# Kernel optimization log

Hardware: AMD Instinct MI355X
Metric: run time of the kernel (lower is better)

## Reference

```python
import jax, jax.numpy as jnp
import numpy as np


def conv2d(x, w, b):
    pad = (w.shape[-1] - 1) // 2
    y = jax.lax.conv_general_dilated(x, w, (1, 1), [(pad, pad), (pad, pad)],
                                     dimension_numbers=('NCHW', 'OIHW', 'NCHW'))
    return y + b[None, :, None, None]


def mish(x):
    return x * jnp.tanh(jax.nn.softplus(x))


def setup_inputs() -> dict:
    key = jax.random.key(0)
    ks = jax.random.split(key, 8)
    B, C, H, W = 8, 16, 256, 256
    s = 0.1
    return dict(
        x=jax.random.normal(ks[0], (B, C, H, W), jnp.float32),
        W1=jax.random.normal(ks[1], (4, 1, 3, 3), jnp.float32) * s,      # conv1: 1->4, k=3
        b1=jnp.zeros((4,), jnp.float32),
        Wred=jax.random.normal(ks[2], (1, 4, 1, 1), jnp.float32) * s,    # involution reduce 4->1
        bred=jnp.zeros((1,), jnp.float32),
        Wspan=jax.random.normal(ks[3], (9, 1, 1, 1), jnp.float32) * s,   # involution span 1->k^2
        bspan=jnp.zeros((9,), jnp.float32),
        W2=jax.random.normal(ks[4], (C, 4 * C, 3, 3), jnp.float32) * s,  # conv2: 4C->C, k=3
        b2=jnp.zeros((C,), jnp.float32),
        Weca=jax.random.normal(ks[5], (3,), jnp.float32) * s,            # ECA 1D conv kernel
    )


def reference(x, W1, b1, Wred, bred, Wspan, bspan, W2, b2, Weca):
    B, C, H, W = x.shape
    H2 = H // 2
    K2 = 9  # 3x3 involution kernel
    # per-channel 1->4 conv + Mish: vectorize the Python channel loop by folding C into batch
    xs = x.reshape(B * C, 1, H, W)
    f = mish(conv2d(xs, W1, b1))                      # (B*C, 4, H, W)
    top, bot = f[:, :, :H2], f[:, :, H2:]             # each (B*C, 4, H2, W)
    # involution2(y1, y2): dynamic per-pixel 3x3 kernel from bottom half, applied to top half
    ker = conv2d(jax.nn.relu(conv2d(bot, Wred, bred)), Wspan, bspan)   # (B*C, 9, H2, W)
    patches = jax.lax.conv_general_dilated_patches(
        top, (3, 3), (1, 1), [(1, 1), (1, 1)],
        dimension_numbers=('NCHW', 'OIHW', 'NCHW'))                    # (B*C, 4*9, H2, W), channel-major
    patches = patches.reshape(B * C, 4, K2, H2, W)
    top_inv = (patches * ker[:, None]).sum(axis=2)                     # (B*C, 4, H2, W)
    # shuffle/concat: out channel-block i = [inv_top_i ; bottom_{(i+1) % C}] along height
    ti = top_inv.reshape(B, C, 4, H2, W)
    bo = bot.reshape(B, C, 4, H2, W)
    shuffled = jnp.concatenate([ti, jnp.roll(bo, -1, axis=1)], axis=3)  # (B, C, 4, H, W)
    shuffled = shuffled.reshape(B, 4 * C, H, W)
    out = mish(conv2d(shuffled, W2, b2))               # (B, C, H, W)
    # ECA: gate from global-avg-pooled `out`, 1D cross-correlation (k=3, pad=1) over channels
    pooled = out.mean(axis=(2, 3))                     # (B, C)
    yp = jnp.pad(pooled, ((0, 0), (1, 1)))
    gate = jax.nn.sigmoid(Weca[0] * yp[:, :-2] + Weca[1] * yp[:, 1:-1] + Weca[2] * yp[:, 2:])
    return x * gate[:, :, None, None]
```

## Files before the change

### kernel.cpp

```cpp
#include <hip/hip_runtime.h>
#include <hip/hip_bf16.h>

#define H 256
#define Wd 256
#define H2 128

typedef unsigned short ushort_t;
typedef __attribute__((ext_vector_type(8))) short short8;
typedef __attribute__((ext_vector_type(4))) float f32x4;
typedef __attribute__((ext_vector_type(2))) float f32x2;

__device__ __forceinline__ float mishf(float v){
  if (v > 15.f) return v;
  float e = __expf(v);
  float w = e*(e+2.f);
  return v * w * __builtin_amdgcn_rcpf(w + 2.f);
}

__device__ __forceinline__ ushort_t f2bf(float f){
  unsigned int u = __float_as_uint(f);
  u += 0x7fffu + ((u >> 16) & 1u);
  return (ushort_t)(u >> 16);
}
__device__ __forceinline__ float bf2f(ushort_t h){
  return __uint_as_float(((unsigned int)h) << 16);
}


__global__ void k0_pack(const float* __restrict__ W2, ushort_t* __restrict__ wpack)
{
  int idx = blockIdx.x*128 + threadIdx.x;
  if (idx >= 1152) return;
  int lane  = idx & 63;
  int s     = (idx >> 6) % 9;
  int khalf = idx / 576;
  int n = lane & 15, g = lane >> 4;
  unsigned int w[4];
#pragma unroll
  for (int h = 0; h < 4; ++h){
    int ch0 = khalf*32 + g*8 + 2*h;
    unsigned lo = f2bf(W2[(n*64 + ch0  )*9 + s]);
    unsigned hi = f2bf(W2[(n*64 + ch0+1)*9 + s]);
    w[h] = lo | (hi << 16);
  }
  *(uint4*)(wpack + (size_t)idx*8) = make_uint4(w[0], w[1], w[2], w[3]);
}

__global__ __launch_bounds__(256) void k12(
    const float* __restrict__ x, const float* __restrict__ W1,
    const float* __restrict__ b1, const float* __restrict__ Wred,
    const float* __restrict__ bred, const float* __restrict__ Wspan,
    const float* __restrict__ bspan, ushort_t* __restrict__ shuf)
{
  __shared__ float xt[20][69];
  __shared__ float xb[18][69];
  __shared__ float ft[4][18][69];

  int bid = blockIdx.x;
  int n   = bid >> 5;
  int t   = bid & 31;
  int itop0 = (t >> 2) * 16;
  int j0    = (t & 3) * 64;
  int tid = threadIdx.x;
  const float* xp = x + (size_t)n * (H*Wd);

  f32x2 w01[9], w23[9], b01, b23, wspb[9];
  float wredr[4];
  float bredr = bred[0];
#pragma unroll
  for (int k=0;k<9;k++){
    w01[k] = f32x2{W1[k], W1[9+k]};
    w23[k] = f32x2{W1[18+k], W1[27+k]};
    wspb[k] = f32x2{Wspan[k], bspan[k]};
  }
  b01 = f32x2{b1[0], b1[1]};
  b23 = f32x2{b1[2], b1[3]};
#pragma unroll
  for (int m=0;m<4;m++) wredr[m] = Wred[m];

  for (int idx=tid; idx<20*68; idx+=256){
    int r = idx/68, c = idx - r*68;
    int row = itop0-2+r, col = j0-2+c;
    xt[r][c] = (row>=0 && col>=0 && col<Wd) ? xp[row*Wd+col] : 0.f;
  }
  for (int idx=tid; idx<18*68; idx+=256){
    int r = idx/68, c = idx - r*68;
    int row = 127+itop0+r, col = j0-2+c;
    xb[r][c] = (row<H && col>=0 && col<Wd) ? xp[row*Wd+col] : 0.f;
  }
  __syncthreads();

  for (int idx=tid; idx<18*66; idx+=256){
    int r = idx/66, c = idx - r*66;
    int frow = itop0-1+r, fcol = j0-1+c;
    bool ok = (frow>=0 && frow<H2 && fcol>=0 && fcol<Wd);
    f32x2 s01 = b01, s23 = b23;
#pragma unroll
    for (int ky=0;ky<3;ky++)
#pragma unroll
      for (int kx=0;kx<3;kx++){
        float xv = xt[r+ky][c+kx];
        f32x2 xv2 = f32x2{xv, xv};
        s01 = xv2*w01[ky*3+kx] + s01;
        s23 = xv2*w23[ky*3+kx] + s23;
      }
    ft[0][r][c] = ok ? mishf(s01.x) : 0.f;
    ft[1][r][c] = ok ? mishf(s01.y) : 0.f;
    ft[2][r][c] = ok ? mishf(s23.x) : 0.f;
    ft[3][r][c] = ok ? mishf(s23.y) : 0.f;
  }

  int lr  = tid >> 4;
  int lc4 = (tid & 15) * 4;
  int trow = itop0 + lr;
  int bq = n >> 4, cq = n & 15;

  float fb[4][4];
  {
    float xv[3][6];
#pragma unroll
    for (int r=0;r<3;r++)
#pragma unroll
      for (int c=0;c<6;c++)
        xv[r][c] = xb[lr+r][lc4+1+c];
#pragma unroll
    for (int p=0;p<4;p++){
      f32x2 s01 = b01, s23 = b23;
#pragma unroll
      for (int ky=0;ky<3;ky++)
#pragma unroll
        for (int kx=0;kx<3;kx++){
          float v = xv[ky][p+kx];
          f32x2 v2 = f32x2{v, v};
          s01 = v2*w01[ky*3+kx] + s01;
          s23 = v2*w23[ky*3+kx] + s23;
        }
      fb[0][p] = mishf(s01.x); fb[1][p] = mishf(s01.y);
      fb[2][p] = mishf(s23.x); fb[3][p] = mishf(s23.y);
    }
  }
  int cdst = (cq + 15) & 15;
  size_t bbase = ((size_t)(bq*16 + cdst))*65536 + (size_t)(128+trow)*256 + j0 + lc4;
#pragma unroll
  for (int p=0;p<4;p++){
    ushort4 hv;
    hv.x = f2bf(fb[0][p]); hv.y = f2bf(fb[1][p]);
    hv.z = f2bf(fb[2][p]); hv.w = f2bf(fb[3][p]);
    *(ushort4*)(shuf + (bbase + p)*4) = hv;
  }
  float gv[4];
#pragma unroll
  for (int p=0;p<4;p++){
    float s = bredr;
#pragma unroll
    for (int m=0;m<4;m++) s = fmaf(fb[m][p], wredr[m], s);
    gv[p] = fmaxf(s, 0.f);
  }

  __syncthreads();

  float o[4][4];
#pragma unroll
  for (int m=0;m<4;m++){
    float fv[3][6];
#pragma unroll
    for (int ky=0;ky<3;ky++)
#pragma unroll
      for (int c=0;c<6;c++)
        fv[ky][c] = ft[m][lr+ky][lc4+c];
#pragma unroll
    for (int p=0;p<4;p++){
      f32x2 ab = f32x2{0.f, 0.f};
#pragma unroll
      for (int ky=0;ky<3;ky++)
#pragma unroll
        for (int kx=0;kx<3;kx++){
          float fvv = fv[ky][p+kx];
          ab = f32x2{fvv, fvv}*wspb[ky*3+kx] + ab;
        }
      o[m][p] = fmaf(gv[p], ab.x, ab.y);
    }
  }
  size_t pbase = ((size_t)(bq*16 + cq))*65536 + (size_t)trow*256 + j0 + lc4;
#pragma unroll
  for (int p=0;p<4;p++){
    ushort4 hv;
    hv.x = f2bf(o[0][p]); hv.y = f2bf(o[1][p]);
    hv.z = f2bf(o[2][p]); hv.w = f2bf(o[3][p]);
    *(ushort4*)(shuf + (pbase + p)*4) = hv;
  }
}

__global__ __launch_bounds__(256) void k3_conv2(
    const ushort_t* __restrict__ shuf, const ushort_t* __restrict__ wpack,
    const float* __restrict__ b2, float* __restrict__ scratch)
{
  __shared__ f32x4 mg[2][8][64];
  __shared__ float pacc[16];

  int bid0 = blockIdx.x;
  int bid  = (bid0 & 7)*256 + (bid0 >> 3);
  int b   = bid >> 8;
  int t   = bid & 255;
  int rb  = t >> 3;
  int cb  = t & 7;
  int tid = threadIdx.x;
  int lane = tid & 63;
  int n = lane & 15;
  int g = lane >> 4;
  int wid = tid >> 6;
  int colhalf = wid & 1;
  int khalf   = wid >> 1;

  if (tid < 16) pacc[tid] = 0.f;

  const short8* wp = (const short8*)wpack + (size_t)khalf*576 + lane;
  short8 afr[9];
#pragma unroll
  for (int s = 0; s < 9; ++s) afr[s] = wp[s*64];

  f32x4 acc[8];
#pragma unroll
  for (int r = 0; r < 8; ++r) acc[r] = f32x4{0.f,0.f,0.f,0.f};

  int r0 = rb*8 - 1;
  int c  = cb*32 - 1 + colhalf*16 + n;
  int p0 = khalf*8 + g*2;
  const ushort_t* sp = shuf + ((size_t)(b*16 + p0))*262144;

#pragma unroll
  for (int hr = 0; hr < 10; ++hr){
    int grow = r0 + hr;
    bool rok = (unsigned)grow < 256u;
    uint2 va[3], vb[3];
#pragma unroll
    for (int kx = 0; kx < 3; ++kx){
      int gcol = c + kx;
      uint2 a = make_uint2(0u,0u), bv = make_uint2(0u,0u);
      if (rok && (unsigned)gcol < 256u){
        const ushort_t* pp = sp + (size_t)(grow*256 + gcol)*4;
        a  = *(const uint2*)pp;
        bv = *(const uint2*)(pp + 262144);
      }
      va[kx] = a; vb[kx] = bv;
    }
#pragma unroll
    for (int kx = 0; kx < 3; ++kx){
      union { uint4 u; short8 s; } cv;
      cv.u = make_uint4(va[kx].x, va[kx].y, vb[kx].x, vb[kx].y);
#pragma unroll
      for (int ky = 0; ky < 3; ++ky){
        int orow = hr - ky;
        if (orow >= 0 && orow < 8){
          acc[orow] = __builtin_amdgcn_mfma_f32_16x16x32_bf16(
              afr[ky*3+kx], cv.s, acc[orow], 0, 0, 0);
        }
      }
    }
  }

  if (khalf == 1){
#pragma unroll
    for (int r = 0; r < 8; ++r) mg[colhalf][r][lane] = acc[r];
  }
  __syncthreads();

  if (khalf == 0){
    float b2v[4];
#pragma unroll
    for (int q = 0; q < 4; ++q) b2v[q] = b2[g*4 + q];
    float po[4] = {0.f, 0.f, 0.f, 0.f};
#pragma unroll
    for (int r = 0; r < 8; ++r){
      f32x4 o = acc[r] + mg[colhalf][r][lane];
#pragma unroll
      for (int q = 0; q < 4; ++q) po[q] += mishf(o[q] + b2v[q]);
    }
#pragma unroll
    for (int q = 0; q < 4; ++q){
#pragma unroll
      for (int mk = 1; mk < 16; mk <<= 1) po[q] += __shfl_xor(po[q], mk);
    }
    if (n == 0){
#pragma unroll
      for (int q = 0; q < 4; ++q) atomicAdd(&pacc[g*4 + q], po[q]);
    }
  }
  __syncthreads();
  if (tid < 16) scratch[bid*16 + tid] = pacc[tid];
}

__global__ void k4_gate(const float* __restrict__ scratch,
                        const float* __restrict__ Weca,
                        float* __restrict__ gate)
{
  __shared__ float rr[16][16];
  __shared__ float pool[16];
  int b = blockIdx.x;
  int t = threadIdx.x;
  int oc = t & 15, ch = t >> 4;
  float s = 0.f;
  for (int u = 0; u < 16; ++u)
    s += scratch[(size_t)(b*256 + ch*16 + u)*16 + oc];
  rr[ch][oc] = s;
  __syncthreads();
  if (t < 16){
    float tot = 0.f;
#pragma unroll
    for (int k = 0; k < 16; ++k) tot += rr[k][t];
    pool[t] = tot * (1.0f/65536.0f);
  }
  __syncthreads();
  if (t < 16){
    float pm = (t > 0)  ? pool[t-1] : 0.f;
    float p0 = pool[t];
    float pp = (t < 15) ? pool[t+1] : 0.f;
    float z = Weca[0]*pm + Weca[1]*p0 + Weca[2]*pp;
    gate[b*16 + t] = 1.f/(1.f + __expf(-z));
  }
}

__global__ __launch_bounds__(256) void k5_scale(
    const f32x4* __restrict__ x4, const float* __restrict__ gate,
    f32x4* __restrict__ out4)
{
  int idx = blockIdx.x*256 + threadIdx.x;
  float g = gate[idx >> 14];
  f32x4 v = x4[idx] * g;
  __builtin_nontemporal_store(v, &out4[idx]);
}

extern "C" void kernel_launch(void* const* d_in, const int* in_sizes, int n_in,
                              void* d_out, int out_size, void* d_ws, size_t ws_size,
                              hipStream_t stream)
{
  const float* x     = (const float*)d_in[0];
  const float* W1    = (const float*)d_in[1];
  const float* b1    = (const float*)d_in[2];
  const float* Wred  = (const float*)d_in[3];
  const float* bred  = (const float*)d_in[4];
  const float* Wspan = (const float*)d_in[5];
  const float* bspan = (const float*)d_in[6];
  const float* W2    = (const float*)d_in[7];
  const float* b2    = (const float*)d_in[8];
  const float* Weca  = (const float*)d_in[9];

  ushort_t* shuf    = (ushort_t*)d_ws;
  float*    gate    = (float*)((char*)d_ws + 67108864);
  ushort_t* wpack   = (ushort_t*)((char*)d_ws + 67108864 + 1024);
  float*    scratch = (float*)d_out;

  k0_pack<<<9, 128, 0, stream>>>(W2, wpack);
  k12    <<<4096, 256, 0, stream>>>(x, W1, b1, Wred, bred, Wspan, bspan, shuf);
  k3_conv2<<<2048, 256, 0, stream>>>(shuf, wpack, b2, scratch);
  k4_gate<<<8, 256, 0, stream>>>(scratch, Weca, gate);
  k5_scale<<<8192, 256, 0, stream>>>((const f32x4*)x, gate, (f32x4*)d_out);
}
```

Before: 90.61 us.

## Vectorize k12 global loads/stores and store top features as packed bf16 in LDS

The input tile loads now use float4 reads with a shifted 4-aligned halo, and the shuffle-buffer writes are widened to two 16-byte stores per thread. The intermediate mish features for the top half are kept in shared memory as packed bf16 pairs, which halves LDS footprint and read traffic. The involution loop is reordered to load the packed features once and unpack them for all four channels. This adds bf16 rounding of intermediate features before the involution, a small precision change, in exchange for lower LDS pressure and fewer memory instructions.

```diff
diff --git a/kernel.cpp b/kernel.cpp
--- a/kernel.cpp
+++ b/kernel.cpp
@@ -24,6 +24,15 @@
 }
 __device__ __forceinline__ float bf2f(ushort_t h){
   return __uint_as_float(((unsigned int)h) << 16);
+}
+__device__ __forceinline__ unsigned packbf(float a, float b){
+  return (unsigned)f2bf(a) | ((unsigned)f2bf(b) << 16);
+}
+__device__ __forceinline__ float lo16(unsigned u){
+  return __uint_as_float(u << 16);
+}
+__device__ __forceinline__ float hi16(unsigned u){
+  return __uint_as_float(u & 0xffff0000u);
 }
 
 
@@ -52,9 +61,9 @@
     const float* __restrict__ bred, const float* __restrict__ Wspan,
     const float* __restrict__ bspan, ushort_t* __restrict__ shuf)
 {
-  __shared__ float xt[20][69];
-  __shared__ float xb[18][69];
-  __shared__ float ft[4][18][69];
+  __shared__ float xt[20][73];
+  __shared__ float xb[18][73];
+  __shared__ unsigned ftp[2][18][69];
 
   int bid = blockIdx.x;
   int n   = bid >> 5;
@@ -78,36 +87,46 @@
 #pragma unroll
   for (int m=0;m<4;m++) wredr[m] = Wred[m];
 
-  for (int idx=tid; idx<20*68; idx+=256){
-    int r = idx/68, c = idx - r*68;
-    int row = itop0-2+r, col = j0-2+c;
-    xt[r][c] = (row>=0 && col>=0 && col<Wd) ? xp[row*Wd+col] : 0.f;
-  }
-  for (int idx=tid; idx<18*68; idx+=256){
-    int r = idx/68, c = idx - r*68;
-    int row = 127+itop0+r, col = j0-2+c;
-    xb[r][c] = (row<H && col>=0 && col<Wd) ? xp[row*Wd+col] : 0.f;
+  for (int idx=tid; idx<360; idx+=256){
+    int r = idx/18, q = idx - r*18;
+    int grow = itop0-2+r, gcol = j0-4+q*4;
+    float4 v = make_float4(0.f,0.f,0.f,0.f);
+    if (grow>=0 && gcol>=0 && gcol<Wd)
+      v = *(const float4*)(xp + (size_t)grow*Wd + gcol);
+    int c0 = q*4;
+    xt[r][c0] = v.x; xt[r][c0+1] = v.y; xt[r][c0+2] = v.z; xt[r][c0+3] = v.w;
+  }
+  for (int idx=tid; idx<324; idx+=256){
+    int r = idx/18, q = idx - r*18;
+    int grow = 127+itop0+r, gcol = j0-4+q*4;
+    float4 v = make_float4(0.f,0.f,0.f,0.f);
+    if (grow<H && gcol>=0 && gcol<Wd)
+      v = *(const float4*)(xp + (size_t)grow*Wd + gcol);
+    int c0 = q*4;
+    xb[r][c0] = v.x; xb[r][c0+1] = v.y; xb[r][c0+2] = v.z; xb[r][c0+3] = v.w;
   }
   __syncthreads();
 
   for (int idx=tid; idx<18*66; idx+=256){
     int r = idx/66, c = idx - r*66;
     int frow = itop0-1+r, fcol = j0-1+c;
-    bool ok = (frow>=0 && frow<H2 && fcol>=0 && fcol<Wd);
-    f32x2 s01 = b01, s23 = b23;
-#pragma unroll
-    for (int ky=0;ky<3;ky++)
-#pragma unroll
-      for (int kx=0;kx<3;kx++){
-        float xv = xt[r+ky][c+kx];
-        f32x2 xv2 = f32x2{xv, xv};
-        s01 = xv2*w01[ky*3+kx] + s01;
-        s23 = xv2*w23[ky*3+kx] + s23;
-      }
-    ft[0][r][c] = ok ? mishf(s01.x) : 0.f;
-    ft[1][r][c] = ok ? mishf(s01.y) : 0.f;
-    ft[2][r][c] = ok ? mishf(s23.x) : 0.f;
-    ft[3][r][c] = ok ? mishf(s23.y) : 0.f;
+    unsigned u01 = 0u, u23 = 0u;
+    if (frow>=0 && frow<H2 && fcol>=0 && fcol<Wd){
+      f32x2 s01 = b01, s23 = b23;
+#pragma unroll
+      for (int ky=0;ky<3;ky++)
+#pragma unroll
+        for (int kx=0;kx<3;kx++){
+          float xv = xt[r+ky][c+kx+2];
+          f32x2 xv2 = f32x2{xv, xv};
+          s01 = xv2*w01[ky*3+kx] + s01;
+          s23 = xv2*w23[ky*3+kx] + s23;
+        }
+      u01 = packbf(mishf(s01.x), mishf(s01.y));
+      u23 = packbf(mishf(s23.x), mishf(s23.y));
+    }
+    ftp[0][r][c] = u01;
+    ftp[1][r][c] = u23;
   }
 
   int lr  = tid >> 4;
@@ -122,7 +141,7 @@
     for (int r=0;r<3;r++)
 #pragma unroll
       for (int c=0;c<6;c++)
-        xv[r][c] = xb[lr+r][lc4+1+c];
+        xv[r][c] = xb[lr+r][lc4+3+c];
 #pragma unroll
     for (int p=0;p<4;p++){
       f32x2 s01 = b01, s23 = b23;
@@ -141,12 +160,13 @@
   }
   int cdst = (cq + 15) & 15;
   size_t bbase = ((size_t)(bq*16 + cdst))*65536 + (size_t)(128+trow)*256 + j0 + lc4;
-#pragma unroll
-  for (int p=0;p<4;p++){
-    ushort4 hv;
-    hv.x = f2bf(fb[0][p]); hv.y = f2bf(fb[1][p]);
-    hv.z = f2bf(fb[2][p]); hv.w = f2bf(fb[3][p]);
-    *(ushort4*)(shuf + (bbase + p)*4) = hv;
+  {
+    unsigned w0 = packbf(fb[0][0], fb[1][0]), w1 = packbf(fb[2][0], fb[3][0]);
+    unsigned w2 = packbf(fb[0][1], fb[1][1]), w3 = packbf(fb[2][1], fb[3][1]);
+    *(uint4*)(shuf + bbase*4) = make_uint4(w0,w1,w2,w3);
+    unsigned w4 = packbf(fb[0][2], fb[1][2]), w5 = packbf(fb[2][2], fb[3][2]);
+    unsigned w6 = packbf(fb[0][3], fb[1][3]), w7 = packbf(fb[2][3], fb[3][3]);
+    *(uint4*)(shuf + (bbase+2)*4) = make_uint4(w4,w5,w6,w7);
   }
   float gv[4];
 #pragma unroll
@@ -159,35 +179,44 @@
 
   __syncthreads();
 
+  unsigned fv0[3][6], fv1[3][6];
+#pragma unroll
+  for (int ky=0;ky<3;ky++)
+#pragma unroll
+    for (int c=0;c<6;c++){
+      fv0[ky][c] = ftp[0][lr+ky][lc4+c];
+      fv1[ky][c] = ftp[1][lr+ky][lc4+c];
+    }
+
   float o[4][4];
 #pragma unroll
-  for (int m=0;m<4;m++){
-    float fv[3][6];
+  for (int p=0;p<4;p++){
+    f32x2 ab0 = f32x2{0.f,0.f}, ab1 = ab0, ab2 = ab0, ab3 = ab0;
 #pragma unroll
     for (int ky=0;ky<3;ky++)
 #pragma unroll
-      for (int c=0;c<6;c++)
-        fv[ky][c] = ft[m][lr+ky][lc4+c];
-#pragma unroll
-    for (int p=0;p<4;p++){
-      f32x2 ab = f32x2{0.f, 0.f};
-#pragma unroll
-      for (int ky=0;ky<3;ky++)
-#pragma unroll
-        for (int kx=0;kx<3;kx++){
-          float fvv = fv[ky][p+kx];
-          ab = f32x2{fvv, fvv}*wspb[ky*3+kx] + ab;
-        }
-      o[m][p] = fmaf(gv[p], ab.x, ab.y);
-    }
+      for (int kx=0;kx<3;kx++){
+        f32x2 w = wspb[ky*3+kx];
+        unsigned u0 = fv0[ky][p+kx], u1 = fv1[ky][p+kx];
+        float a = lo16(u0), b = hi16(u0), c2 = lo16(u1), d = hi16(u1);
+        ab0 = f32x2{a,a}*w + ab0;
+        ab1 = f32x2{b,b}*w + ab1;
+        ab2 = f32x2{c2,c2}*w + ab2;
+        ab3 = f32x2{d,d}*w + ab3;
+      }
+    o[0][p] = fmaf(gv[p], ab0.x, ab0.y);
+    o[1][p] = fmaf(gv[p], ab1.x, ab1.y);
+    o[2][p] = fmaf(gv[p], ab2.x, ab2.y);
+    o[3][p] = fmaf(gv[p], ab3.x, ab3.y);
   }
   size_t pbase = ((size_t)(bq*16 + cq))*65536 + (size_t)trow*256 + j0 + lc4;
-#pragma unroll
-  for (int p=0;p<4;p++){
-    ushort4 hv;
-    hv.x = f2bf(o[0][p]); hv.y = f2bf(o[1][p]);
-    hv.z = f2bf(o[2][p]); hv.w = f2bf(o[3][p]);
-    *(ushort4*)(shuf + (pbase + p)*4) = hv;
+  {
+    unsigned w0 = packbf(o[0][0], o[1][0]), w1 = packbf(o[2][0], o[3][0]);
+    unsigned w2 = packbf(o[0][1], o[1][1]), w3 = packbf(o[2][1], o[3][1]);
+    *(uint4*)(shuf + pbase*4) = make_uint4(w0,w1,w2,w3);
+    unsigned w4 = packbf(o[0][2], o[1][2]), w5 = packbf(o[2][2], o[3][2]);
+    unsigned w6 = packbf(o[0][3], o[1][3]), w7 = packbf(o[2][3], o[3][3]);
+    *(uint4*)(shuf + (pbase+2)*4) = make_uint4(w4,w5,w6,w7);
   }
 }
 
```

Result: faster. 85.45 us (-5.7%).
